# Kernel tuning notes

Hardware: AMD Instinct MI355X
Metric: run time of the kernel (lower is better)

The kernel has to match this reference:

```python
import jax, jax.numpy as jnp
import numpy as np

SCALE, R_MAX, ALPHA = 16, 8, 2.0
HL, WL, C_FEAT = 16, 16, 384
HH, WH = HL * SCALE, WL * SCALE


def bilinear_resize(img, out_h, out_w):
    """PyTorch F.interpolate(mode='bilinear', align_corners=False, antialias=False).
    img: [..., H, W] -> [..., out_h, out_w]."""
    H, W = img.shape[-2], img.shape[-1]
    ys = jnp.maximum((jnp.arange(out_h, dtype=jnp.float32) + 0.5) * (H / out_h) - 0.5, 0.0)
    xs = jnp.maximum((jnp.arange(out_w, dtype=jnp.float32) + 0.5) * (W / out_w) - 0.5, 0.0)
    y0 = jnp.floor(ys).astype(jnp.int32)
    x0 = jnp.floor(xs).astype(jnp.int32)
    y1 = jnp.minimum(y0 + 1, H - 1)
    x1 = jnp.minimum(x0 + 1, W - 1)
    wy = (ys - y0)[:, None]
    wx = (xs - x0)[None, :]
    g = lambda yi, xi: img[..., yi[:, None], xi[None, :]]
    return ((1 - wy) * (1 - wx) * g(y0, x0) + (1 - wy) * wx * g(y0, x1)
            + wy * (1 - wx) * g(y1, x0) + wy * wx * g(y1, x1))


def jbu_forward(feat_lr, guide_hr, sx_raw, sy_raw, th_raw, sr_raw):
    C, Hl, Wl = feat_lr.shape[1], feat_lr.shape[2], feat_lr.shape[3]
    Hh, Wh = guide_hr.shape[2], guide_hr.shape[3]
    scale, R_max, alpha = SCALE, R_MAX, ALPHA
    NEG = -1e30  # finite stand-in for -inf (keeps grads NaN-free)

    # parameter transforms from the module
    sx = jnp.exp(sx_raw[0, 0])
    sy = jnp.exp(sy_raw[0, 0])
    th = jnp.pi * jnp.tanh(th_raw[0, 0])
    sr = jnp.exp(sr_raw[0, 0])

    Y, X = jnp.meshgrid(jnp.arange(Hh, dtype=jnp.float32),
                        jnp.arange(Wh, dtype=jnp.float32), indexing='ij')
    u = (Y + 0.5) / scale - 0.5
    v = (X + 0.5) / scale - 0.5
    uc = jnp.clip(jnp.round(u), 0, Hl - 1).astype(jnp.int32)
    vc = jnp.clip(jnp.round(v), 0, Wl - 1).astype(jnp.int32)

    sigma_eff_hr = bilinear_resize(jnp.maximum(sx, sy), Hh, Wh)
    R_map = jnp.clip(jnp.ceil(alpha * sigma_eff_hr), 1.0, float(R_max))  # [Hh,Wh]

    offs = jnp.arange(-R_max, R_max + 1, dtype=jnp.int32)
    dYg, dXg = jnp.meshgrid(offs, offs, indexing='ij')
    dY = dYg.reshape(-1)[:, None, None]  # [N,1,1]
    dX = dXg.reshape(-1)[:, None, None]

    Ui = jnp.clip(uc[None] + dY, 0, Hl - 1)  # [N,Hh,Wh]
    Vi = jnp.clip(vc[None] + dX, 0, Wl - 1)
    idx = Ui * Wl + Vi                       # flat LR index per (neighbor, HR pixel)
    gat = lambda mp: mp.reshape(-1)[idx]

    sxg = jnp.maximum(gat(sx), 1e-6)
    syg = jnp.maximum(gat(sy), 1e-6)
    thg = gat(th)
    srg = jnp.maximum(gat(sr), 1e-6)

    dx = X[None] - ((Vi.astype(jnp.float32) + 0.5) * scale - 0.5)
    dyv = Y[None] - ((Ui.astype(jnp.float32) + 0.5) * scale - 0.5)
    ct, st = jnp.cos(thg), jnp.sin(thg)
    a = dx * ct + dyv * st
    b = -dx * st + dyv * ct

    guide_lr = bilinear_resize(guide_hr[0], Hl, Wl)  # [3,Hl,Wl]
    g_diff2 = sum((guide_hr[0, c][None] - gat(guide_lr[c])) ** 2 for c in range(3))

    log_w = (-a * a / (2 * sxg ** 2 + 1e-8)
             - b * b / (2 * syg ** 2 + 1e-8)
             - g_diff2 / (2.0 * srg ** 2 + 1e-8))  # [N,Hh,Wh]

    mask = (dY * dY + dX * dX).astype(jnp.float32) <= R_map[None] ** 2
    log_w = jnp.where(mask, log_w, NEG)

    # numerically stable softmax over neighbors (== online-softmax result)
    m = log_w.max(axis=0)
    s = jnp.exp(log_w - m[None])  # masked entries underflow to 0
    den = s.sum(axis=0)           # [Hh,Wh]

    # num[c,h,w] = sum_n s[n,h,w] * feat[idx[n,h,w], c]
    # scatter neighbor weights by LR pixel, then one GEMM with the LR features
    N = idx.shape[0]
    idx2 = idx.reshape(N, Hh * Wh)
    cols = jnp.arange(Hh * Wh, dtype=jnp.int32)[None, :]
    acc = jnp.zeros((Hl * Wl, Hh * Wh), jnp.float32).at[idx2, cols].add(s.reshape(N, -1))
    feat_flat = feat_lr[0].reshape(C, Hl * Wl)  # [C, P]
    num = jnp.einsum('cp,pq->cq', feat_flat, acc).reshape(C, Hh, Wh)

    return (num / jnp.maximum(den, 1e-8)[None])[None]  # [1,C,Hh,Wh]


def setup_inputs() -> dict:
    key = jax.random.key(0)
    k1, k2, k3, k4, k5, k6 = jax.random.split(key, 6)
    feat_lr = jax.random.normal(k1, (1, C_FEAT, HL, WL), jnp.float32)
    guide_hr = jax.random.uniform(k2, (1, 3, HH, WH), dtype=jnp.float32)
    log_sigma = float(np.log(16.0))
    log_sigma_r = float(np.log(0.12))
    sx_raw = log_sigma + 0.1 * jax.random.normal(k3, (1, 1, HL, WL), jnp.float32)
    sy_raw = log_sigma + 0.1 * jax.random.normal(k4, (1, 1, HL, WL), jnp.float32)
    th_raw = 0.1 * jax.random.normal(k5, (1, 1, HL, WL), jnp.float32)
    sr_raw = log_sigma_r + 0.1 * jax.random.normal(k6, (1, 1, HL, WL), jnp.float32)
    return {"feat_lr": feat_lr, "guide_hr": guide_hr, "sx_raw": sx_raw,
            "sy_raw": sy_raw, "th_raw": th_raw, "sr_raw": sr_raw}


def reference(feat_lr, guide_hr, sx_raw, sy_raw, th_raw, sr_raw):
    return jbu_forward(feat_lr, guide_hr, sx_raw, sy_raw, th_raw, sr_raw)
```

## Files before the change

### kernel.cpp

```cpp
#include <hip/hip_runtime.h>
#include <math.h>

#define NEG_BIG  (-1e30f)
#define NEG_H16  (-60000.0f)

typedef _Float16 half8  __attribute__((ext_vector_type(8)));
typedef _Float16 half2v __attribute__((ext_vector_type(2)));
typedef float    floatx4 __attribute__((ext_vector_type(4)));

__global__ __launch_bounds__(256) void setup_all(
    const float* __restrict__ feat, const float* __restrict__ guide,
    const float* __restrict__ sx_raw, const float* __restrict__ sy_raw,
    const float* __restrict__ th_raw, const float* __restrict__ sr_raw,
    _Float16* __restrict__ feat16, float4* __restrict__ PQ,
    float4* __restrict__ PG)
{
    const int b = blockIdx.x, t = threadIdx.x;
    if (b < 384) {
        int i = b*256 + t;
        feat16[i] = (_Float16)feat[i];
        return;
    }
    float sx = expf(sx_raw[t]);
    float sy = expf(sy_raw[t]);
    float th = 3.14159265358979323846f * tanhf(th_raw[t]);
    float sr = expf(sr_raw[t]);
    float sxg = fmaxf(sx, 1e-6f), syg = fmaxf(sy, 1e-6f), srg = fmaxf(sr, 1e-6f);
    float iA = 1.f / (2.f*sxg*sxg + 1e-8f);
    float iB = 1.f / (2.f*syg*syg + 1e-8f);
    float iC = 1.f / (2.f*srg*srg + 1e-8f);
    float ct = cosf(th), st = sinf(th);
    float A2 = iA*ct*ct + iB*st*st;
    float B2 = 2.f*ct*st*(iA - iB);
    float C2 = iA*st*st + iB*ct*ct;
    PQ[t] = make_float4(A2, B2, C2, iC);
    int i = t >> 4, j = t & 15;
    int y0 = 16*i + 7, x0 = 16*j + 7;
    float g[3];
#pragma unroll
    for (int c = 0; c < 3; ++c) {
        const float* gp = guide + c*65536;
        g[c] = 0.25f*(gp[y0*256 + x0]     + gp[y0*256 + x0 + 1] +
                      gp[(y0+1)*256 + x0] + gp[(y0+1)*256 + x0 + 1]);
    }
    PG[t] = make_float4(g[0], g[1], g[2], fmaxf(sx, sy));
}

__global__ __launch_bounds__(256, 4) void jbu_main(
    const float* __restrict__ guide, const _Float16* __restrict__ feat16,
    const float4* __restrict__ PQ, const float4* __restrict__ PG,
    float* __restrict__ out)
{
    __shared__ float4 sPQ[256];
    __shared__ float4 sPG[256];
    __shared__ _Float16 LCh[4096];
    __shared__ __align__(16) _Float16 Wb[32][256];
    __shared__ float redM[4][32];
    __shared__ float redD[4][32];

    const int t = threadIdx.x;
    sPQ[t] = PQ[t];
    sPG[t] = PG[t];

    const int q    = t & 31;
    const int grp  = t >> 5;
    const int wv   = t >> 6;
    const int Y    = blockIdx.y;
    const int X0   = blockIdx.x << 5;
    const int X    = X0 + q;
    const float Yf = (float)Y, Xf = (float)X;
    const int uc   = Y >> 4;
    const int vc0  = X0 >> 4;

    {
        const int Pu  = t >> 4;
        const int col = t & 15;
        const int Rt  = (col >> 1) + 1;
        const int vc  = vc0 + (col & 1);
        const int R2  = Rt * Rt;
        int ylo = (Pu == 0)  ? -8 : (Pu - uc);
        int yhi = (Pu == 15) ?  8 : (Pu - uc);
        ylo = max(ylo, -8); yhi = min(yhi, 8);
        int cnt[16];
#pragma unroll
        for (int Pv = 1; Pv < 15; ++Pv) {
            int d = Pv - vc;
            int lim = R2 - d*d;
            int c = 0;
            if (lim >= 0 && ylo <= yhi) {
                int s = (int)sqrtf((float)lim);
                c = max(0, min(yhi, s) - max(ylo, -s) + 1);
            }
            cnt[Pv] = c;
        }
        cnt[0] = 0;
        if (-vc >= -8) {
            for (int dY = ylo; dY <= yhi; ++dY) {
                int lim = R2 - dY*dY;
                if (lim >= 0) {
                    int r = (int)sqrtf((float)lim);
                    cnt[0] += max(0, min(-vc, r) + r + 1);
                }
            }
        }
        cnt[15] = 0;
        if (15 - vc <= 8) {
            for (int dY = ylo; dY <= yhi; ++dY) {
                int lim = R2 - dY*dY;
                if (lim >= 0) {
                    int r = (int)sqrtf((float)lim);
                    cnt[15] += max(0, r - max(15 - vc, -r) + 1);
                }
            }
        }
#pragma unroll
        for (int Pv = 0; Pv < 16; ++Pv)
            LCh[(Pu*16 + Pv)*16 + col] = (_Float16)
                ((cnt[Pv] > 0) ? __logf((float)cnt[Pv]) : NEG_H16);
    }
    __syncthreads();

    float u = (Yf + 0.5f)*0.0625f - 0.5f;
    float v = (Xf + 0.5f)*0.0625f - 0.5f;
    float ysc = fmaxf(u, 0.f), xsc = fmaxf(v, 0.f);
    int y0 = (int)ysc, x0 = (int)xsc;
    int y1 = min(y0 + 1, 15), x1 = min(x0 + 1, 15);
    float wy = ysc - (float)y0, wx = xsc - (float)x0;
    float s00 = sPG[y0*16 + x0].w, s01 = sPG[y0*16 + x1].w;
    float s10 = sPG[y1*16 + x0].w, s11 = sPG[y1*16 + x1].w;
    float sig = (1.f - wy)*((1.f - wx)*s00 + wx*s01)
              +        wy *((1.f - wx)*s10 + wx*s11);
    float Rf = fminf(fmaxf(ceilf(2.f*sig), 1.f), 8.f);
    const int colq = ((int)Rf - 1)*2 + (q >> 4);

    const float g0 = guide[          (Y << 8) + X];
    const float g1 = guide[ 65536 + ((Y << 8) + X)];
    const float g2 = guide[131072 + ((Y << 8) + X)];

    const int pbase = grp << 5;
    const float dy0 = Yf - (16.f*(float)(grp*2) + 7.5f);
    float lw[32];
    float mloc = NEG_BIG;
#pragma unroll
    for (int pi = 0; pi < 32; ++pi) {
        int p = pbase + pi;
        float4 Q = sPQ[p];
        float4 G = sPG[p];
        float dy = (pi < 16) ? dy0 : (dy0 - 16.f);
        float dx = Xf - (16.f*(float)(pi & 15) + 7.5f);
        float d0 = g0 - G.x, d1 = g1 - G.y, d2 = g2 - G.z;
        float gd = d0*d0 + d1*d1 + d2*d2;
        float quad = Q.x*(dx*dx) + Q.y*(dx*dy) + Q.z*(dy*dy) + Q.w*gd;
        float w = (float)LCh[p*16 + colq] - quad;
        lw[pi] = w;
        mloc = fmaxf(mloc, w);
    }
    mloc = fmaxf(mloc, __shfl_xor(mloc, 32, 64));
    redM[wv][q] = mloc;
    __syncthreads();
    float m = fmaxf(fmaxf(redM[0][q], redM[1][q]),
                    fmaxf(redM[2][q], redM[3][q]));

    float dloc = 0.f;
#pragma unroll
    for (int pi = 0; pi < 32; pi += 2) {
        int p = pbase + pi;
        float e0 = __expf(lw[pi]     - m);
        float e1 = __expf(lw[pi + 1] - m);
        half2v hh; hh[0] = (_Float16)e0; hh[1] = (_Float16)e1;
        int chunk = ((p >> 3) ^ q) & 31;
        *(half2v*)&Wb[q][chunk*8 + (p & 7)] = hh;
        dloc += (float)hh[0] + (float)hh[1];
    }
    dloc += __shfl_xor(dloc, 32, 64);
    redD[wv][q] = dloc;
    __syncthreads();

    const int lane = t & 63;
    const int mrow = lane & 15;
    const int quad = lane >> 4;
    const int c0   = wv * 96;

    float idv[2];
#pragma unroll
    for (int nt = 0; nt < 2; ++nt) {
        int pix = nt*16 + mrow;
        float den = redD[0][pix] + redD[1][pix] + redD[2][pix] + redD[3][pix];
        idv[nt] = 1.f / fmaxf(den, 1e-8f);
    }

    floatx4 acc[6][2] = {};
    const _Float16* fbase = feat16 + (c0 + mrow)*256 + quad*8;

#pragma unroll
    for (int ks = 0; ks < 8; ++ks) {
        half8 a[6];
#pragma unroll
        for (int mt = 0; mt < 6; ++mt)
            a[mt] = *(const half8*)(fbase + mt*16*256 + ks*32);
        half8 b[2];
#pragma unroll
        for (int nt = 0; nt < 2; ++nt) {
            int pix = nt*16 + mrow;
            int chunk = ((ks*4 + quad) ^ pix) & 31;
            b[nt] = *(const half8*)(&Wb[pix][chunk*8]);
        }
#pragma unroll
        for (int mt = 0; mt < 6; ++mt)
#pragma unroll
            for (int nt = 0; nt < 2; ++nt)
                acc[mt][nt] = __builtin_amdgcn_mfma_f32_16x16x32_f16(
                    a[mt], b[nt], acc[mt][nt], 0, 0, 0);
    }

    const int outbase = (Y << 8) + X0;
#pragma unroll
    for (int nt = 0; nt < 2; ++nt) {
#pragma unroll
        for (int mt = 0; mt < 6; ++mt) {
            int crow = c0 + mt*16 + quad*4;
            float* o = out + (size_t)crow*65536 + outbase + nt*16 + mrow;
#pragma unroll
            for (int r = 0; r < 4; ++r)
                o[(size_t)r*65536] = acc[mt][nt][r] * idv[nt];
        }
    }
}

extern "C" void kernel_launch(void* const* d_in, const int* in_sizes, int n_in,
                              void* d_out, int out_size, void* d_ws, size_t ws_size,
                              hipStream_t stream)
{
    const float* feat   = (const float*)d_in[0];
    const float* guide  = (const float*)d_in[1];
    const float* sx_raw = (const float*)d_in[2];
    const float* sy_raw = (const float*)d_in[3];
    const float* th_raw = (const float*)d_in[4];
    const float* sr_raw = (const float*)d_in[5];
    float* out = (float*)d_out;

    _Float16* feat16 = (_Float16*)d_ws;
    float4*   PQ     = (float4*)((char*)d_ws + 196608);
    float4*   PG     = (float4*)((char*)d_ws + 196608 + 4096);

    setup_all<<<385, 256, 0, stream>>>(feat, guide, sx_raw, sy_raw, th_raw,
                                       sr_raw, feat16, PQ, PG);
    jbu_main<<<dim3(8, 256), 256, 0, stream>>>(guide, feat16, PQ, PG, out);
}
```

Measured before the change: 161.5 us.

## Precompute log-count tables in setup, expand quadratic weights, coalesce output stores via LDS

The per-block log-count table computation moves into 128 extra setup blocks, so the main kernel only copies a precomputed 8 KB table into shared memory. The range term is expanded algebraically so per-LR-pixel constants (2*iC*g and -iC*|g|^2) are precomputed and the inner loop becomes a chain of FMAs with dx^2 and dx*dy hoisted per column. Output is staged through LDS (reusing the LCh buffer) so each wave writes contiguous float4 rows instead of scattered scalar stores. The cost is extra workspace traffic for the table, reading sigma directly from global memory, and an extra LDS round trip in the epilogue.

```diff
diff --git a/kernel.cpp b/kernel.cpp
--- a/kernel.cpp
+++ b/kernel.cpp
@@ -12,8 +12,9 @@
     const float* __restrict__ feat, const float* __restrict__ guide,
     const float* __restrict__ sx_raw, const float* __restrict__ sy_raw,
     const float* __restrict__ th_raw, const float* __restrict__ sr_raw,
-    _Float16* __restrict__ feat16, float4* __restrict__ PQ,
-    float4* __restrict__ PG)
+    _Float16* __restrict__ feat16, float4* __restrict__ PA,
+    float4* __restrict__ PB, float* __restrict__ PS,
+    _Float16* __restrict__ LCtab)
 {
     const int b = blockIdx.x, t = threadIdx.x;
     if (b < 384) {
@@ -21,47 +22,98 @@
         feat16[i] = (_Float16)feat[i];
         return;
     }
-    float sx = expf(sx_raw[t]);
-    float sy = expf(sy_raw[t]);
-    float th = 3.14159265358979323846f * tanhf(th_raw[t]);
-    float sr = expf(sr_raw[t]);
-    float sxg = fmaxf(sx, 1e-6f), syg = fmaxf(sy, 1e-6f), srg = fmaxf(sr, 1e-6f);
-    float iA = 1.f / (2.f*sxg*sxg + 1e-8f);
-    float iB = 1.f / (2.f*syg*syg + 1e-8f);
-    float iC = 1.f / (2.f*srg*srg + 1e-8f);
-    float ct = cosf(th), st = sinf(th);
-    float A2 = iA*ct*ct + iB*st*st;
-    float B2 = 2.f*ct*st*(iA - iB);
-    float C2 = iA*st*st + iB*ct*ct;
-    PQ[t] = make_float4(A2, B2, C2, iC);
-    int i = t >> 4, j = t & 15;
-    int y0 = 16*i + 7, x0 = 16*j + 7;
-    float g[3];
-#pragma unroll
-    for (int c = 0; c < 3; ++c) {
-        const float* gp = guide + c*65536;
-        g[c] = 0.25f*(gp[y0*256 + x0]     + gp[y0*256 + x0 + 1] +
-                      gp[(y0+1)*256 + x0] + gp[(y0+1)*256 + x0 + 1]);
-    }
-    PG[t] = make_float4(g[0], g[1], g[2], fmaxf(sx, sy));
+    if (b == 384) {
+        float sx = expf(sx_raw[t]);
+        float sy = expf(sy_raw[t]);
+        float th = 3.14159265358979323846f * tanhf(th_raw[t]);
+        float sr = expf(sr_raw[t]);
+        float sxg = fmaxf(sx, 1e-6f), syg = fmaxf(sy, 1e-6f), srg = fmaxf(sr, 1e-6f);
+        float iA = 1.f / (2.f*sxg*sxg + 1e-8f);
+        float iB = 1.f / (2.f*syg*syg + 1e-8f);
+        float iC = 1.f / (2.f*srg*srg + 1e-8f);
+        float ct = cosf(th), st = sinf(th);
+        float A2 = iA*ct*ct + iB*st*st;
+        float B2 = 2.f*ct*st*(iA - iB);
+        float C2 = iA*st*st + iB*ct*ct;
+        PA[t] = make_float4(-A2, -B2, -C2, -iC);
+        int i = t >> 4, j = t & 15;
+        int y0 = 16*i + 7, x0 = 16*j + 7;
+        float g[3];
+#pragma unroll
+        for (int c = 0; c < 3; ++c) {
+            const float* gp = guide + c*65536;
+            g[c] = 0.25f*(gp[y0*256 + x0]     + gp[y0*256 + x0 + 1] +
+                          gp[(y0+1)*256 + x0] + gp[(y0+1)*256 + x0 + 1]);
+        }
+        PB[t] = make_float4(2.f*iC*g[0], 2.f*iC*g[1], 2.f*iC*g[2],
+                            -iC*(g[0]*g[0] + g[1]*g[1] + g[2]*g[2]));
+        PS[t] = fmaxf(sx, sy);
+        return;
+    }
+    const int tb  = b - 385;
+    const int uc  = tb >> 3;
+    const int vc0 = (tb & 7) << 1;
+    const int Pu  = t >> 4;
+    const int col = t & 15;
+    const int Rt  = (col >> 1) + 1;
+    const int vc  = vc0 + (col & 1);
+    const int R2  = Rt * Rt;
+    int ylo = (Pu == 0)  ? -8 : (Pu - uc);
+    int yhi = (Pu == 15) ?  8 : (Pu - uc);
+    ylo = max(ylo, -8); yhi = min(yhi, 8);
+    int cnt[16];
+#pragma unroll
+    for (int Pv = 1; Pv < 15; ++Pv) {
+        int d = Pv - vc;
+        int lim = R2 - d*d;
+        int c = 0;
+        if (lim >= 0 && ylo <= yhi) {
+            int s = (int)sqrtf((float)lim);
+            c = max(0, min(yhi, s) - max(ylo, -s) + 1);
+        }
+        cnt[Pv] = c;
+    }
+    cnt[0] = 0;
+    if (-vc >= -8) {
+        for (int dY = ylo; dY <= yhi; ++dY) {
+            int lim = R2 - dY*dY;
+            if (lim >= 0) {
+                int r = (int)sqrtf((float)lim);
+                cnt[0] += max(0, min(-vc, r) + r + 1);
+            }
+        }
+    }
+    cnt[15] = 0;
+    if (15 - vc <= 8) {
+        for (int dY = ylo; dY <= yhi; ++dY) {
+            int lim = R2 - dY*dY;
+            if (lim >= 0) {
+                int r = (int)sqrtf((float)lim);
+                cnt[15] += max(0, r - max(15 - vc, -r) + 1);
+            }
+        }
+    }
+    _Float16* dst = LCtab + (size_t)tb * 4096;
+#pragma unroll
+    for (int Pv = 0; Pv < 16; ++Pv)
+        dst[(Pu*16 + Pv)*16 + col] = (_Float16)
+            ((cnt[Pv] > 0) ? __logf((float)cnt[Pv]) : NEG_H16);
 }
 
 __global__ __launch_bounds__(256, 4) void jbu_main(
     const float* __restrict__ guide, const _Float16* __restrict__ feat16,
-    const float4* __restrict__ PQ, const float4* __restrict__ PG,
+    const float4* __restrict__ PA, const float4* __restrict__ PB,
+    const float* __restrict__ PS, const _Float16* __restrict__ LCtab,
     float* __restrict__ out)
 {
-    __shared__ float4 sPQ[256];
-    __shared__ float4 sPG[256];
-    __shared__ _Float16 LCh[4096];
+    __shared__ float4 sPA[256];
+    __shared__ float4 sPB[256];
+    __shared__ __align__(16) _Float16 LCh[4096];
     __shared__ __align__(16) _Float16 Wb[32][256];
     __shared__ float redM[4][32];
     __shared__ float redD[4][32];
 
     const int t = threadIdx.x;
-    sPQ[t] = PQ[t];
-    sPG[t] = PG[t];
-
     const int q    = t & 31;
     const int grp  = t >> 5;
     const int wv   = t >> 6;
@@ -70,55 +122,15 @@
     const int X    = X0 + q;
     const float Yf = (float)Y, Xf = (float)X;
     const int uc   = Y >> 4;
-    const int vc0  = X0 >> 4;
-
+
+    sPA[t] = PA[t];
+    sPB[t] = PB[t];
     {
-        const int Pu  = t >> 4;
-        const int col = t & 15;
-        const int Rt  = (col >> 1) + 1;
-        const int vc  = vc0 + (col & 1);
-        const int R2  = Rt * Rt;
-        int ylo = (Pu == 0)  ? -8 : (Pu - uc);
-        int yhi = (Pu == 15) ?  8 : (Pu - uc);
-        ylo = max(ylo, -8); yhi = min(yhi, 8);
-        int cnt[16];
-#pragma unroll
-        for (int Pv = 1; Pv < 15; ++Pv) {
-            int d = Pv - vc;
-            int lim = R2 - d*d;
-            int c = 0;
-            if (lim >= 0 && ylo <= yhi) {
-                int s = (int)sqrtf((float)lim);
-                c = max(0, min(yhi, s) - max(ylo, -s) + 1);
-            }
-            cnt[Pv] = c;
-        }
-        cnt[0] = 0;
-        if (-vc >= -8) {
-            for (int dY = ylo; dY <= yhi; ++dY) {
-                int lim = R2 - dY*dY;
-                if (lim >= 0) {
-                    int r = (int)sqrtf((float)lim);
-                    cnt[0] += max(0, min(-vc, r) + r + 1);
-                }
-            }
-        }
-        cnt[15] = 0;
-        if (15 - vc <= 8) {
-            for (int dY = ylo; dY <= yhi; ++dY) {
-                int lim = R2 - dY*dY;
-                if (lim >= 0) {
-                    int r = (int)sqrtf((float)lim);
-                    cnt[15] += max(0, r - max(15 - vc, -r) + 1);
-                }
-            }
-        }
-#pragma unroll
-        for (int Pv = 0; Pv < 16; ++Pv)
-            LCh[(Pu*16 + Pv)*16 + col] = (_Float16)
-                ((cnt[Pv] > 0) ? __logf((float)cnt[Pv]) : NEG_H16);
-    }
-    __syncthreads();
+        const float4* Lsrc =
+            (const float4*)(LCtab + (size_t)(uc*8 + blockIdx.x) * 4096);
+        ((float4*)LCh)[t]       = Lsrc[t];
+        ((float4*)LCh)[t + 256] = Lsrc[t + 256];
+    }
 
     float u = (Yf + 0.5f)*0.0625f - 0.5f;
     float v = (Xf + 0.5f)*0.0625f - 0.5f;
@@ -126,8 +138,8 @@
     int y0 = (int)ysc, x0 = (int)xsc;
     int y1 = min(y0 + 1, 15), x1 = min(x0 + 1, 15);
     float wy = ysc - (float)y0, wx = xsc - (float)x0;
-    float s00 = sPG[y0*16 + x0].w, s01 = sPG[y0*16 + x1].w;
-    float s10 = sPG[y1*16 + x0].w, s11 = sPG[y1*16 + x1].w;
+    float s00 = PS[y0*16 + x0], s01 = PS[y0*16 + x1];
+    float s10 = PS[y1*16 + x0], s11 = PS[y1*16 + x1];
     float sig = (1.f - wy)*((1.f - wx)*s00 + wx*s01)
               +        wy *((1.f - wx)*s10 + wx*s11);
     float Rf = fminf(fmaxf(ceilf(2.f*sig), 1.f), 8.f);
@@ -136,24 +148,38 @@
     const float g0 = guide[          (Y << 8) + X];
     const float g1 = guide[ 65536 + ((Y << 8) + X)];
     const float g2 = guide[131072 + ((Y << 8) + X)];
+    const float g2s = g0*g0 + g1*g1 + g2*g2;
+
+    __syncthreads();
 
     const int pbase = grp << 5;
-    const float dy0 = Yf - (16.f*(float)(grp*2) + 7.5f);
+    const float dy0  = Yf - (32.f*(float)grp + 7.5f);
+    const float dy1  = dy0 - 16.f;
+    const float dy20 = dy0*dy0, dy21 = dy1*dy1;
     float lw[32];
     float mloc = NEG_BIG;
 #pragma unroll
-    for (int pi = 0; pi < 32; ++pi) {
-        int p = pbase + pi;
-        float4 Q = sPQ[p];
-        float4 G = sPG[p];
-        float dy = (pi < 16) ? dy0 : (dy0 - 16.f);
-        float dx = Xf - (16.f*(float)(pi & 15) + 7.5f);
-        float d0 = g0 - G.x, d1 = g1 - G.y, d2 = g2 - G.z;
-        float gd = d0*d0 + d1*d1 + d2*d2;
-        float quad = Q.x*(dx*dx) + Q.y*(dx*dy) + Q.z*(dy*dy) + Q.w*gd;
-        float w = (float)LCh[p*16 + colq] - quad;
-        lw[pi] = w;
-        mloc = fmaxf(mloc, w);
+    for (int col = 0; col < 16; ++col) {
+        float dx    = Xf - (16.f*(float)col + 7.5f);
+        float dx2   = dx*dx;
+        float dxdy0 = dx*dy0, dxdy1 = dx*dy1;
+#pragma unroll
+        for (int row = 0; row < 2; ++row) {
+            int pi = row*16 + col;
+            int p  = pbase + pi;
+            float4 A = sPA[p];
+            float4 B = sPB[p];
+            float w = fmaf(B.x, g0, B.w);
+            w = fmaf(B.y, g1, w);
+            w = fmaf(B.z, g2, w);
+            w = fmaf(A.w, g2s, w);
+            w = fmaf(A.x, dx2, w);
+            w = fmaf(A.y, row ? dxdy1 : dxdy0, w);
+            w = fmaf(A.z, row ? dy21  : dy20,  w);
+            w += (float)LCh[p*16 + colq];
+            lw[pi] = w;
+            mloc = fmaxf(mloc, w);
+        }
     }
     mloc = fmaxf(mloc, __shfl_xor(mloc, 32, 64));
     redM[wv][q] = mloc;
@@ -213,16 +239,22 @@
                     a[mt], b[nt], acc[mt][nt], 0, 0, 0);
     }
 
-    const int outbase = (Y << 8) + X0;
-#pragma unroll
-    for (int nt = 0; nt < 2; ++nt) {
-#pragma unroll
-        for (int mt = 0; mt < 6; ++mt) {
-            int crow = c0 + mt*16 + quad*4;
-            float* o = out + (size_t)crow*65536 + outbase + nt*16 + mrow;
+    float* Sf = (float*)LCh + (wv << 9);
+    const int sch = lane >> 3;
+    const int spg = lane & 7;
+    const int outcol = (Y << 8) + X0;
+#pragma unroll
+    for (int mt = 0; mt < 6; ++mt) {
+#pragma unroll
+        for (int nt = 0; nt < 2; ++nt)
 #pragma unroll
             for (int r = 0; r < 4; ++r)
-                o[(size_t)r*65536] = acc[mt][nt][r] * idv[nt];
+                Sf[(quad*4 + r)*32 + nt*16 + mrow] = acc[mt][nt][r] * idv[nt];
+#pragma unroll
+        for (int j = 0; j < 2; ++j) {
+            float4 vv = *(const float4*)&Sf[(j*8 + sch)*32 + spg*4];
+            *(float4*)(out + (size_t)(c0 + mt*16 + j*8 + sch)*65536
+                           + outcol + spg*4) = vv;
         }
     }
 }
@@ -239,11 +271,15 @@
     const float* sr_raw = (const float*)d_in[5];
     float* out = (float*)d_out;
 
-    _Float16* feat16 = (_Float16*)d_ws;
-    float4*   PQ     = (float4*)((char*)d_ws + 196608);
-    float4*   PG     = (float4*)((char*)d_ws + 196608 + 4096);
-
-    setup_all<<<385, 256, 0, stream>>>(feat, guide, sx_raw, sy_raw, th_raw,
-                                       sr_raw, feat16, PQ, PG);
-    jbu_main<<<dim3(8, 256), 256, 0, stream>>>(guide, feat16, PQ, PG, out);
+    char* ws = (char*)d_ws;
+    _Float16* feat16 = (_Float16*)ws;
+    float4*   PA     = (float4*)(ws + 196608);
+    float4*   PB     = (float4*)(ws + 200704);
+    float*    PS     = (float*)(ws + 204800);
+    _Float16* LCtab  = (_Float16*)(ws + 205824);
+
+    setup_all<<<513, 256, 0, stream>>>(feat, guide, sx_raw, sy_raw, th_raw,
+                                       sr_raw, feat16, PA, PB, PS, LCtab);
+    jbu_main<<<dim3(8, 256), 256, 0, stream>>>(guide, feat16, PA, PB, PS,
+                                               LCtab, out);
 }
```

Result: no change. 158.6 us (-1.8%).
